# Performance work log

Hardware: AMD Instinct MI355X
Metric: run time of the kernel (lower is better)

## Reference

```python
import jax, jax.numpy as jnp
import numpy as np

# Standard FP4 E2M1 lookup table (nvfp4-style): sign bit in nibble MSB.
FP4_LUT = jnp.array([0.0, 0.5, 1.0, 1.5, 2.0, 3.0, 4.0, 6.0,
                     -0.0, -0.5, -1.0, -1.5, -2.0, -3.0, -4.0, -6.0],
                    dtype=jnp.float32)


def dequant_fp4(packed_i32, scales, group_size):
    """packed_i32: [K/8, N] int32 (8 fp4 nibbles per word, low nibble first);
    scales: [K/group_size, N]. Returns dense fp32 weight [K, N]."""
    w = jax.lax.bitcast_convert_type(packed_i32, jnp.uint32)  # [K/8, N]
    # Unpack nibbles along the reduction axis: nibble i -> row 8*r + i.
    nib = jnp.stack([(w >> jnp.uint32(4 * i)) & jnp.uint32(0xF) for i in range(8)],
                    axis=1)                                    # [K/8, 8, N]
    K = nib.shape[0] * 8
    nib = nib.reshape(K, w.shape[1])                           # [K, N]
    vals = FP4_LUT[nib]                                        # [K, N]
    s = jnp.repeat(scales, group_size, axis=0)                 # [K, N]
    return vals * s


def setup_inputs() -> dict:
    key = jax.random.key(0)
    k1, k2, k3, k4, k5, k6 = jax.random.split(key, 6)
    tokens, H, I, G = 4096, 2048, 5632, 128
    return {
        "hidden": jax.random.normal(k1, (tokens, H), dtype=jnp.float32),
        "moe_output": jax.random.normal(k2, (tokens, H), dtype=jnp.float32),
        "gate_up_weights": jax.random.randint(k3, (H // 8, 2 * I), 0, 2147483647, dtype=jnp.int32),
        "gate_up_scales": jax.random.uniform(k4, (H // G, 2 * I), dtype=jnp.float32, minval=0.01, maxval=0.1),
        "down_weights": jax.random.randint(k5, (I // 8, H), 0, 2147483647, dtype=jnp.int32),
        "down_scales": jax.random.uniform(k6, (I // G, H), dtype=jnp.float32, minval=0.01, maxval=0.1),
        "group_size": G,
    }


def reference(hidden, moe_output, gate_up_weights, gate_up_scales,
              down_weights, down_scales, group_size):
    # Shared-expert SwiGLU FFN with FP4 group-quantized weights, fused residual add.
    W_gu = dequant_fp4(gate_up_weights, gate_up_scales, group_size)  # [H, 2I]
    gu = hidden @ W_gu                                               # [T, 2I]
    I = gu.shape[1] // 2
    gate, up = gu[:, :I], gu[:, I:]
    act = jax.nn.silu(gate) * up                                     # [T, I]
    W_d = dequant_fp4(down_weights, down_scales, group_size)         # [I, H]
    return moe_output + act @ W_d                                    # [T, H]
```

## Files before the change

kernel.cpp:

```cpp
#include <hip/hip_runtime.h>
#include <hip/hip_fp16.h>
#include <stdint.h>

#define TOKENS 4096
#define HDIM   2048
#define IDIM   5632
#define BM 128
#define BN 128
#define BK 64

#define G1_NP  11264
#define G1_KSB (G1_NP * 64)

typedef _Float16 f16x8 __attribute__((ext_vector_type(8)));
typedef float    f32x4 __attribute__((ext_vector_type(4)));

__device__ __forceinline__ uint32_t dec2(uint32_t z, uint32_t s2u) {
    uint32_t sgn = (z << 12) & 0x80008000u;
    uint32_t h   = ((z << 9) & 0x0E000E00u) | sgn;
    __half2 hv = __builtin_bit_cast(__half2, h);
    __half2 sv = __builtin_bit_cast(__half2, s2u);
    __half2 r  = __hmul2(hv, sv);
    return __builtin_bit_cast(uint32_t, r);
}
__device__ __forceinline__ int4 dec8(uint32_t w, uint32_t s2u) {
    int4 d;
    d.x = (int)dec2( w        & 0x000F000Fu, s2u);
    d.y = (int)dec2((w >> 4)  & 0x000F000Fu, s2u);
    d.z = (int)dec2((w >> 8)  & 0x000F000Fu, s2u);
    d.w = (int)dec2((w >> 12) & 0x000F000Fu, s2u);
    return d;
}
__device__ __forceinline__ uint32_t scale_s2u(float sc) {
    uint16_t hs = __builtin_bit_cast(uint16_t, __float2half(sc * 16384.0f));
    return (uint32_t)hs * 0x00010001u;
}
__device__ __forceinline__ uint32_t packh(float lo, float hi) {
    __half2 h2 = __halves2half2(__float2half(lo), __float2half(hi));
    return __builtin_bit_cast(uint32_t, h2);
}
__device__ __forceinline__ void gl_lds16(const void* g, void* l) {
    __builtin_amdgcn_global_load_lds(
        (const __attribute__((address_space(1))) uint32_t*)g,
        (__attribute__((address_space(3))) uint32_t*)l, 16, 0, 0);
}

__global__ __launch_bounds__(256) void convert_hidden(
    const float* __restrict__ src, __half* __restrict__ dst)
{
    int idx = blockIdx.x * 256 + threadIdx.x;
    const float4* s = (const float4*)src + (size_t)idx * 2;
    float4 a = s[0], b = s[1];
    int4 v;
    v.x = (int)packh(a.x, b.x);
    v.y = (int)packh(a.y, b.y);
    v.z = (int)packh(a.z, b.z);
    v.w = (int)packh(a.w, b.w);
    *((int4*)dst + idx) = v;
}

__global__ __launch_bounds__(256) void dequant_wgu7(
    const uint32_t* __restrict__ W, const float* __restrict__ S,
    __half* __restrict__ Bt)
{
    const int kt = blockIdx.y;
    const int t  = threadIdx.x;
    const int np = blockIdx.x * 32 + (t >> 3);
    const int j  = t & 7;
    const int sc = (np >> 6) * 32 + (np & 31) + (((np >> 5) & 1) ? IDIM : 0);
    uint32_t s2u = scale_s2u(S[(size_t)(kt >> 1) * (2 * IDIM) + sc]);
    uint32_t w   = W[(size_t)(kt * 8 + j) * (2 * IDIM) + sc];
    int4 d = dec8(w, s2u);
    *(int4*)(Bt + (size_t)kt * G1_KSB + (size_t)np * 64 + j * 8) = d;
}

__global__ __launch_bounds__(256, 4) void gemm1_s(
    const __half* __restrict__ A, const __half* __restrict__ Bt,
    __half* __restrict__ act)
{
    __shared__ __half Alds[BM * 64];
    __shared__ __half Blds[BN * 64];
    const int tid  = threadIdx.x;
    const int lane = tid & 63;
    const int wid  = tid >> 6;
    const int wm = wid >> 1, wn = wid & 1;
    const int m0 = blockIdx.y * BM;
    const int n0 = blockIdx.x * BN;

    f32x4 acc[4][4];
    #pragma unroll
    for (int i = 0; i < 4; ++i)
        #pragma unroll
        for (int j = 0; j < 4; ++j) acc[i][j] = f32x4{0.f, 0.f, 0.f, 0.f};

    const __half* srcA[4];
    const __half* srcB[4];
    #pragma unroll
    for (int i = 0; i < 4; ++i) {
        int u = i * 256 + tid, row = u >> 3, s = u & 7, sl = s ^ (row & 7);
        srcA[i] = A  + (size_t)(m0 + row) * HDIM + sl * 8;
        srcB[i] = Bt + (size_t)(n0 + row) * 64 + sl * 8;
    }

    int aoff[4][2], boff[4][2];
    #pragma unroll
    for (int f = 0; f < 4; ++f)
        #pragma unroll
        for (int ks = 0; ks < 2; ++ks) {
            int kb = ks * 4 + (lane >> 4);
            int ra = wm * 64 + f * 16 + (lane & 15);
            int rb = wn * 64 + f * 16 + (lane & 15);
            aoff[f][ks] = ra * 128 + ((kb ^ (ra & 7)) << 4);
            boff[f][ks] = rb * 128 + ((kb ^ (rb & 7)) << 4);
        }

    for (int kt = 0; kt < HDIM / 64; ++kt) {
        #pragma unroll
        for (int i = 0; i < 4; ++i) {
            int u = i * 256 + tid;
            gl_lds16(srcA[i], (char*)Alds + u * 16);
            gl_lds16(srcB[i], (char*)Blds + u * 16);
            srcA[i] += 64;
            srcB[i] += G1_KSB;
        }
        __syncthreads();
        #pragma unroll
        for (int ks = 0; ks < 2; ++ks) {
            f16x8 af[4], bf[4];
            #pragma unroll
            for (int f = 0; f < 4; ++f) {
                af[f] = *(const f16x8*)((const char*)Alds + aoff[f][ks]);
                bf[f] = *(const f16x8*)((const char*)Blds + boff[f][ks]);
            }
            #pragma unroll
            for (int mi = 0; mi < 4; ++mi)
                #pragma unroll
                for (int ni = 0; ni < 4; ++ni)
                    acc[mi][ni] = __builtin_amdgcn_mfma_f32_16x16x32_f16(af[mi], bf[ni], acc[mi][ni], 0, 0, 0);
        }
        __syncthreads();
    }

    const int pairbase = ((n0 + wn * 64) >> 6) * 32;
    #pragma unroll
    for (int mi = 0; mi < 4; ++mi) {
        #pragma unroll
        for (int q = 0; q < 2; ++q) {
            int gcol = pairbase + q * 16 + (lane & 15);
            int colstore = (gcol & ~7) | (((gcol & 3) << 1) | ((gcol >> 2) & 1));
            #pragma unroll
            for (int r = 0; r < 4; ++r) {
                int m = m0 + wm * 64 + mi * 16 + (lane >> 4) * 4 + r;
                float gv = acc[mi][q][r];
                float uv = acc[mi][q + 2][r];
                float sig = 1.0f / (1.0f + __expf(-gv));
                act[(size_t)m * IDIM + colstore] = __float2half(gv * sig * uv);
            }
        }
    }
}

__global__ __launch_bounds__(256, 2) void gemm1_silu(
    const __half* __restrict__ A, const uint32_t* __restrict__ W,
    const float* __restrict__ S, __half* __restrict__ act)
{
    __shared__ __half Alds[BM * BK];
    __shared__ __half Blds[2][BN * BK];
    const int tid  = threadIdx.x;
    const int lane = tid & 63;
    const int wid  = tid >> 6;
    const int wm = wid >> 1, wn = wid & 1;
    const int m0 = blockIdx.y * BM;
    const int c0 = blockIdx.x * BN;

    f32x4 accg[4][4], accu[4][4];
    #pragma unroll
    for (int i = 0; i < 4; ++i)
        #pragma unroll
        for (int j = 0; j < 4; ++j) {
            accg[i][j] = f32x4{0.f, 0.f, 0.f, 0.f};
            accu[i][j] = f32x4{0.f, 0.f, 0.f, 0.f};
        }

    const int c = tid & 127;
    const int rbase = (tid >> 7) * 4;

    for (int kt = 0; kt < HDIM / BK; ++kt) {
        const int k0 = kt * BK;
        #pragma unroll
        for (int i = 0; i < 4; ++i) {
            int u = tid + i * 256;
            int row = u >> 3, kb = u & 7;
            int4 v = *(const int4*)(A + (size_t)(m0 + row) * HDIM + k0 + kb * 8);
            *(int4*)((char*)Alds + row * 128 + ((kb ^ (row & 7)) << 4)) = v;
        }
        const int g = k0 >> 7;
        #pragma unroll
        for (int p = 0; p < 2; ++p) {
            const int ncol = (p ? IDIM : 0) + c0 + c;
            uint32_t s2u = scale_s2u(S[(size_t)g * (2 * IDIM) + ncol]);
            #pragma unroll
            for (int i = 0; i < 4; ++i) {
                int rl = rbase + i;
                uint32_t w = W[(size_t)(kt * 8 + rl) * (2 * IDIM) + ncol];
                int4 d = dec8(w, s2u);
                *(int4*)((char*)&Blds[p][0] + c * 128 + ((rl ^ (c & 7)) << 4)) = d;
            }
        }
        __syncthreads();
        #pragma unroll
        for (int ks = 0; ks < 2; ++ks) {
            f16x8 af[4], bg[4], bu[4];
            const int kb = ks * 4 + (lane >> 4);
            #pragma unroll
            for (int mi = 0; mi < 4; ++mi) {
                int m = wm * 64 + mi * 16 + (lane & 15);
                af[mi] = *(const f16x8*)((const char*)Alds + m * 128 + ((kb ^ (m & 7)) << 4));
            }
            #pragma unroll
            for (int ni = 0; ni < 4; ++ni) {
                int n = wn * 64 + ni * 16 + (lane & 15);
                bg[ni] = *(const f16x8*)((const char*)&Blds[0][0] + n * 128 + ((kb ^ (n & 7)) << 4));
                bu[ni] = *(const f16x8*)((const char*)&Blds[1][0] + n * 128 + ((kb ^ (n & 7)) << 4));
            }
            #pragma unroll
            for (int mi = 0; mi < 4; ++mi)
                #pragma unroll
                for (int ni = 0; ni < 4; ++ni) {
                    accg[mi][ni] = __builtin_amdgcn_mfma_f32_16x16x32_f16(af[mi], bg[ni], accg[mi][ni], 0, 0, 0);
                    accu[mi][ni] = __builtin_amdgcn_mfma_f32_16x16x32_f16(af[mi], bu[ni], accu[mi][ni], 0, 0, 0);
                }
        }
        __syncthreads();
    }
    #pragma unroll
    for (int mi = 0; mi < 4; ++mi) {
        #pragma unroll
        for (int ni = 0; ni < 4; ++ni) {
            int nlog = c0 + wn * 64 + ni * 16 + (lane & 15);
            int ncol = (nlog & ~7) | (((nlog & 3) << 1) | ((nlog >> 2) & 1));
            #pragma unroll
            for (int r = 0; r < 4; ++r) {
                int m = m0 + wm * 64 + mi * 16 + (lane >> 4) * 4 + r;
                float gv = accg[mi][ni][r];
                float uv = accu[mi][ni][r];
                float sig = 1.0f / (1.0f + __expf(-gv));
                act[(size_t)m * IDIM + ncol] = __float2half(gv * sig * uv);
            }
        }
    }
}

__global__ __launch_bounds__(256, 2) void gemm2_add(
    const __half* __restrict__ A, const uint32_t* __restrict__ W,
    const float* __restrict__ S, const float* __restrict__ moe,
    float* __restrict__ out)
{
    __shared__ __half Alds[BM * BK];
    __shared__ __half Blds[BN * BK];
    const int tid  = threadIdx.x;
    const int lane = tid & 63;
    const int wid  = tid >> 6;
    const int wm = wid >> 1, wn = wid & 1;
    const int m0 = blockIdx.y * BM;
    const int n0 = blockIdx.x * BN;

    f32x4 acc[4][4];
    #pragma unroll
    for (int i = 0; i < 4; ++i)
        #pragma unroll
        for (int j = 0; j < 4; ++j) acc[i][j] = f32x4{0.f, 0.f, 0.f, 0.f};

    const int c = tid & 127;
    const int rbase = (tid >> 7) * 4;

    int aoff[4][2], boff[4][2];
    #pragma unroll
    for (int f = 0; f < 4; ++f)
        #pragma unroll
        for (int ks = 0; ks < 2; ++ks) {
            int kb = ks * 4 + (lane >> 4);
            int ra = wm * 64 + f * 16 + (lane & 15);
            int rb = wn * 64 + f * 16 + (lane & 15);
            aoff[f][ks] = ra * 128 + ((kb ^ (ra & 7)) << 4);
            boff[f][ks] = rb * 128 + ((kb ^ (rb & 7)) << 4);
        }

    for (int kt = 0; kt < IDIM / BK; ++kt) {
        const int k0 = kt * BK;
        #pragma unroll
        for (int i = 0; i < 4; ++i) {
            int u = tid + i * 256;
            int row = u >> 3, kb = u & 7;
            int4 v = *(const int4*)(A + (size_t)(m0 + row) * IDIM + k0 + kb * 8);
            *(int4*)((char*)Alds + row * 128 + ((kb ^ (row & 7)) << 4)) = v;
        }
        {
            const int g = k0 >> 7;
            const int ncol = n0 + c;
            uint32_t s2u = scale_s2u(S[(size_t)g * HDIM + ncol]);
            #pragma unroll
            for (int i = 0; i < 4; ++i) {
                int rl = rbase + i;
                uint32_t w = W[(size_t)(kt * 8 + rl) * HDIM + ncol];
                int4 d = dec8(w, s2u);
                *(int4*)((char*)Blds + c * 128 + ((rl ^ (c & 7)) << 4)) = d;
            }
        }
        __syncthreads();
        #pragma unroll
        for (int ks = 0; ks < 2; ++ks) {
            f16x8 af[4], bf[4];
            #pragma unroll
            for (int f = 0; f < 4; ++f) {
                af[f] = *(const f16x8*)((const char*)Alds + aoff[f][ks]);
                bf[f] = *(const f16x8*)((const char*)Blds + boff[f][ks]);
            }
            #pragma unroll
            for (int mi = 0; mi < 4; ++mi)
                #pragma unroll
                for (int ni = 0; ni < 4; ++ni)
                    acc[mi][ni] = __builtin_amdgcn_mfma_f32_16x16x32_f16(af[mi], bf[ni], acc[mi][ni], 0, 0, 0);
        }
        __syncthreads();
    }
    #pragma unroll
    for (int mi = 0; mi < 4; ++mi) {
        #pragma unroll
        for (int ni = 0; ni < 4; ++ni) {
            int n = n0 + wn * 64 + ni * 16 + (lane & 15);
            #pragma unroll
            for (int r = 0; r < 4; ++r) {
                int m = m0 + wm * 64 + mi * 16 + (lane >> 4) * 4 + r;
                out[(size_t)m * HDIM + n] = moe[(size_t)m * HDIM + n] + acc[mi][ni][r];
            }
        }
    }
}

extern "C" void kernel_launch(void* const* d_in, const int* in_sizes, int n_in,
                              void* d_out, int out_size, void* d_ws, size_t ws_size,
                              hipStream_t stream) {
    const float*    hidden = (const float*)d_in[0];
    const float*    moe    = (const float*)d_in[1];
    const uint32_t* wgu    = (const uint32_t*)d_in[2];
    const float*    sgu    = (const float*)d_in[3];
    const uint32_t* wd     = (const uint32_t*)d_in[4];
    const float*    sd     = (const float*)d_in[5];
    float* out = (float*)d_out;

    const size_t sz_hidden = (size_t)TOKENS * HDIM * 2;
    const size_t sz_act    = (size_t)TOKENS * IDIM * 2;
    const size_t sz_wgu16  = (size_t)HDIM * 2 * IDIM * 2;

    __half* hidden_f16 = (__half*)d_ws;
    __half* act        = (__half*)((char*)d_ws + sz_hidden);
    __half* wgu16      = (__half*)((char*)d_ws + sz_hidden + sz_act);

    const size_t need_g1 = sz_hidden + sz_act + sz_wgu16;

    convert_hidden<<<dim3(TOKENS * HDIM / 8 / 256), dim3(256), 0, stream>>>(hidden, hidden_f16);

    if (ws_size >= need_g1) {
        dequant_wgu7<<<dim3(G1_NP / 32, 32), dim3(256), 0, stream>>>(wgu, sgu, wgu16);
        gemm1_s<<<dim3(G1_NP / BN, TOKENS / BM), dim3(256), 0, stream>>>(hidden_f16, wgu16, act);
    } else {
        gemm1_silu<<<dim3(IDIM / BN, TOKENS / BM), dim3(256), 0, stream>>>(hidden_f16, wgu, sgu, act);
    }

    gemm2_add<<<dim3(HDIM / BN, TOKENS / BM), dim3(256), 0, stream>>>(act, wd, sd, moe, out);
}
```

Baseline: 326.0 us.

## Rewrite gate-up GEMM as 256x256 tile, 8-wave double-buffered phased pipeline

Replaces the 128x128, 4-wave single-buffered gemm1 with a 256x256 tile kernel using 8 waves, double-buffered LDS and a four-phase schedule. Global-to-LDS loads for tile kt+2 are interleaved with the MFMA phases, and s_setprio raises priority around the MFMA blocks. The aim is to hide load latency, cut the barrier stalls of the old load-then-compute loop and raise data reuse per tile. In exchange it needs 128KB LDS and many more accumulator registers, which allows only one block per CU, and gives a smaller grid (44x16 blocks).

Result: no change. 321.6 us (-1.4%).

```diff
diff --git a/kernel.cpp b/kernel.cpp
--- a/kernel.cpp
+++ b/kernel.cpp
@@ -74,83 +74,154 @@
     *(int4*)(Bt + (size_t)kt * G1_KSB + (size_t)np * 64 + j * 8) = d;
 }
 
-__global__ __launch_bounds__(256, 4) void gemm1_s(
+__global__ __launch_bounds__(512, 1) void gemm1_8ph2(
     const __half* __restrict__ A, const __half* __restrict__ Bt,
     __half* __restrict__ act)
 {
-    __shared__ __half Alds[BM * 64];
-    __shared__ __half Blds[BN * 64];
+    __shared__ __half Al[2][256 * 64];
+    __shared__ __half Bl[2][256 * 64];
     const int tid  = threadIdx.x;
     const int lane = tid & 63;
     const int wid  = tid >> 6;
-    const int wm = wid >> 1, wn = wid & 1;
-    const int m0 = blockIdx.y * BM;
-    const int n0 = blockIdx.x * BN;
-
-    f32x4 acc[4][4];
-    #pragma unroll
-    for (int i = 0; i < 4; ++i)
-        #pragma unroll
-        for (int j = 0; j < 4; ++j) acc[i][j] = f32x4{0.f, 0.f, 0.f, 0.f};
+    const int wm   = wid >> 2;
+    const int wn   = wid & 3;
+
+    const int m0 = blockIdx.y * 256;
+    const int n0 = blockIdx.x * 256;
 
     const __half* srcA[4];
     const __half* srcB[4];
     #pragma unroll
     for (int i = 0; i < 4; ++i) {
-        int u = i * 256 + tid, row = u >> 3, s = u & 7, sl = s ^ (row & 7);
+        int u = i * 512 + tid, row = u >> 3, s = u & 7, sl = s ^ (row & 7);
         srcA[i] = A  + (size_t)(m0 + row) * HDIM + sl * 8;
         srcB[i] = Bt + (size_t)(n0 + row) * 64 + sl * 8;
     }
 
-    int aoff[4][2], boff[4][2];
-    #pragma unroll
-    for (int f = 0; f < 4; ++f)
-        #pragma unroll
-        for (int ks = 0; ks < 2; ++ks) {
-            int kb = ks * 4 + (lane >> 4);
-            int ra = wm * 64 + f * 16 + (lane & 15);
-            int rb = wn * 64 + f * 16 + (lane & 15);
-            aoff[f][ks] = ra * 128 + ((kb ^ (ra & 7)) << 4);
-            boff[f][ks] = rb * 128 + ((kb ^ (rb & 7)) << 4);
-        }
-
-    for (int kt = 0; kt < HDIM / 64; ++kt) {
-        #pragma unroll
-        for (int i = 0; i < 4; ++i) {
-            int u = i * 256 + tid;
-            gl_lds16(srcA[i], (char*)Alds + u * 16);
-            gl_lds16(srcB[i], (char*)Blds + u * 16);
-            srcA[i] += 64;
-            srcB[i] += G1_KSB;
-        }
-        __syncthreads();
-        #pragma unroll
-        for (int ks = 0; ks < 2; ++ks) {
-            f16x8 af[4], bf[4];
-            #pragma unroll
-            for (int f = 0; f < 4; ++f) {
-                af[f] = *(const f16x8*)((const char*)Alds + aoff[f][ks]);
-                bf[f] = *(const f16x8*)((const char*)Blds + boff[f][ks]);
-            }
-            #pragma unroll
-            for (int mi = 0; mi < 4; ++mi)
-                #pragma unroll
-                for (int ni = 0; ni < 4; ++ni)
-                    acc[mi][ni] = __builtin_amdgcn_mfma_f32_16x16x32_f16(af[mi], bf[ni], acc[mi][ni], 0, 0, 0);
-        }
-        __syncthreads();
+    auto stageA = [&](int buf, int kt) {
+        #pragma unroll
+        for (int i = 0; i < 4; ++i)
+            gl_lds16(srcA[i] + (size_t)kt * 64, (char*)&Al[buf][0] + (i * 512 + tid) * 16);
+    };
+    auto stageB = [&](int buf, int kt) {
+        #pragma unroll
+        for (int i = 0; i < 4; ++i)
+            gl_lds16(srcB[i] + (size_t)kt * G1_KSB, (char*)&Bl[buf][0] + (i * 512 + tid) * 16);
+    };
+
+    f32x4 acc[8][4];
+    #pragma unroll
+    for (int i = 0; i < 8; ++i)
+        #pragma unroll
+        for (int j = 0; j < 4; ++j) acc[i][j] = f32x4{0.f, 0.f, 0.f, 0.f};
+
+    const int rA0 = wm * 128 + (lane & 15);
+    const int rB0 = wn * 64  + (lane & 15);
+    const int kb0 = lane >> 4;
+
+    stageB(0, 0); stageA(0, 0);
+    stageB(1, 1); stageA(1, 1);
+    asm volatile("s_waitcnt vmcnt(8)" ::: "memory");
+    asm volatile("s_barrier" ::: "memory");
+
+    f16x8 a[4][2], b[4][2];
+    for (int kt = 0; kt < 32; ++kt) {
+        const int cur = kt & 1;
+        const __half* Ac = &Al[cur][0];
+        const __half* Bc = &Bl[cur][0];
+        const bool st = kt < 30;
+
+        #pragma unroll
+        for (int mi = 0; mi < 4; ++mi)
+            #pragma unroll
+            for (int kk = 0; kk < 2; ++kk) {
+                int r = rA0 + mi * 16;
+                a[mi][kk] = *(const f16x8*)&Ac[r * 64 + (((kb0 + kk * 4) ^ (r & 7)) << 3)];
+            }
+        #pragma unroll
+        for (int ni = 0; ni < 2; ++ni)
+            #pragma unroll
+            for (int kk = 0; kk < 2; ++kk) {
+                int r = rB0 + ni * 16;
+                b[ni][kk] = *(const f16x8*)&Bc[r * 64 + (((kb0 + kk * 4) ^ (r & 7)) << 3)];
+            }
+        asm volatile("s_barrier" ::: "memory");
+        __builtin_amdgcn_s_setprio(1);
+        #pragma unroll
+        for (int mi = 0; mi < 4; ++mi)
+            #pragma unroll
+            for (int ni = 0; ni < 2; ++ni)
+                #pragma unroll
+                for (int kk = 0; kk < 2; ++kk)
+                    acc[mi][ni] = __builtin_amdgcn_mfma_f32_16x16x32_f16(a[mi][kk], b[ni][kk], acc[mi][ni], 0, 0, 0);
+        __builtin_amdgcn_s_setprio(0);
+        asm volatile("s_barrier" ::: "memory");
+
+        #pragma unroll
+        for (int ni = 2; ni < 4; ++ni)
+            #pragma unroll
+            for (int kk = 0; kk < 2; ++kk) {
+                int r = rB0 + ni * 16;
+                b[ni][kk] = *(const f16x8*)&Bc[r * 64 + (((kb0 + kk * 4) ^ (r & 7)) << 3)];
+            }
+        asm volatile("s_barrier" ::: "memory");
+        __builtin_amdgcn_s_setprio(1);
+        #pragma unroll
+        for (int mi = 0; mi < 4; ++mi)
+            #pragma unroll
+            for (int ni = 2; ni < 4; ++ni)
+                #pragma unroll
+                for (int kk = 0; kk < 2; ++kk)
+                    acc[mi][ni] = __builtin_amdgcn_mfma_f32_16x16x32_f16(a[mi][kk], b[ni][kk], acc[mi][ni], 0, 0, 0);
+        __builtin_amdgcn_s_setprio(0);
+        asm volatile("s_barrier" ::: "memory");
+
+        #pragma unroll
+        for (int mi = 0; mi < 4; ++mi)
+            #pragma unroll
+            for (int kk = 0; kk < 2; ++kk) {
+                int r = rA0 + (mi + 4) * 16;
+                a[mi][kk] = *(const f16x8*)&Ac[r * 64 + (((kb0 + kk * 4) ^ (r & 7)) << 3)];
+            }
+        if (st) stageB(cur, kt + 2);
+        asm volatile("s_barrier" ::: "memory");
+        __builtin_amdgcn_s_setprio(1);
+        #pragma unroll
+        for (int mi = 0; mi < 4; ++mi)
+            #pragma unroll
+            for (int ni = 2; ni < 4; ++ni)
+                #pragma unroll
+                for (int kk = 0; kk < 2; ++kk)
+                    acc[mi + 4][ni] = __builtin_amdgcn_mfma_f32_16x16x32_f16(a[mi][kk], b[ni][kk], acc[mi + 4][ni], 0, 0, 0);
+        __builtin_amdgcn_s_setprio(0);
+        asm volatile("s_barrier" ::: "memory");
+
+        if (st) stageA(cur, kt + 2);
+        asm volatile("s_barrier" ::: "memory");
+        __builtin_amdgcn_s_setprio(1);
+        #pragma unroll
+        for (int mi = 0; mi < 4; ++mi)
+            #pragma unroll
+            for (int ni = 0; ni < 2; ++ni)
+                #pragma unroll
+                for (int kk = 0; kk < 2; ++kk)
+                    acc[mi + 4][ni] = __builtin_amdgcn_mfma_f32_16x16x32_f16(a[mi][kk], b[ni][kk], acc[mi + 4][ni], 0, 0, 0);
+        __builtin_amdgcn_s_setprio(0);
+        if (st) asm volatile("s_waitcnt vmcnt(8)" ::: "memory");
+        else    asm volatile("s_waitcnt vmcnt(0)" ::: "memory");
+        asm volatile("s_barrier" ::: "memory");
     }
 
     const int pairbase = ((n0 + wn * 64) >> 6) * 32;
     #pragma unroll
-    for (int mi = 0; mi < 4; ++mi) {
+    for (int mi = 0; mi < 8; ++mi) {
         #pragma unroll
         for (int q = 0; q < 2; ++q) {
             int gcol = pairbase + q * 16 + (lane & 15);
             int colstore = (gcol & ~7) | (((gcol & 3) << 1) | ((gcol >> 2) & 1));
             #pragma unroll
             for (int r = 0; r < 4; ++r) {
-                int m = m0 + wm * 64 + mi * 16 + (lane >> 4) * 4 + r;
+                int m = m0 + wm * 128 + mi * 16 + (lane >> 4) * 4 + r;
                 float gv = acc[mi][q][r];
                 float uv = acc[mi][q + 2][r];
                 float sig = 1.0f / (1.0f + __expf(-gv));
@@ -363,7 +434,7 @@
 
     if (ws_size >= need_g1) {
         dequant_wgu7<<<dim3(G1_NP / 32, 32), dim3(256), 0, stream>>>(wgu, sgu, wgu16);
-        gemm1_s<<<dim3(G1_NP / BN, TOKENS / BM), dim3(256), 0, stream>>>(hidden_f16, wgu16, act);
+        gemm1_8ph2<<<dim3(G1_NP / 256, TOKENS / 256), dim3(512), 0, stream>>>(hidden_f16, wgu16, act);
     } else {
         gemm1_silu<<<dim3(IDIM / BN, TOKENS / BM), dim3(256), 0, stream>>>(hidden_f16, wgu, sgu, act);
     }
```
